# Kernel optimization log

Measured on AMD Instinct MI355X. Metric: run time of the kernel, lower is better.

## Reference

```python
import jax, jax.numpy as jnp
import numpy as np
from jax import lax

NMS_THR = 0.5
MIN_HEIGHT = 50.0
PULL_W = 1.0
PUSH_W = 1.0
EPS = 1e-6

B, N, G = 8, 2048, 64


def setup_inputs() -> dict:
    key = jax.random.key(0)
    k1, k2, k3, k4, k5, k6, k7 = jax.random.split(key, 7)
    # proposals: valid boxes (x1,y1,x2,y2) plus score in column 4
    cxy = jax.random.uniform(k1, (B, N, 2), minval=0.0, maxval=1000.0)
    wh = jax.random.uniform(k2, (B, N, 2), minval=10.0, maxval=200.0)
    scores = jax.random.uniform(k3, (B, N, 1))
    proposal_list = jnp.concatenate([cxy - wh / 2, cxy + wh / 2, scores], axis=-1)
    # gt boxes: heights straddle MIN_HEIGHT so the push branch is exercised
    gxy = jax.random.uniform(k4, (B, G, 2), minval=0.0, maxval=1000.0)
    gwh = jax.random.uniform(k5, (B, G, 2), minval=20.0, maxval=160.0)
    gt_bboxes = jnp.concatenate([gxy - gwh / 2, gxy + gwh / 2], axis=-1)
    # assignment ids in [-1, G); -1 = negative anchor
    anchor_gt_inds = jax.random.randint(k6, (B, N), -1, G, dtype=jnp.int32)
    gt_inds = jax.random.randint(k7, (B, N), -1, G, dtype=jnp.int32)  # dead arg in original
    return {"gt_inds": gt_inds, "anchor_gt_inds": anchor_gt_inds,
            "gt_bboxes": gt_bboxes, "proposal_list": proposal_list}


def bbox_overlaps(a, b):
    # a: [A,4], b: [B,4] -> IoU [A,B]
    area_a = (a[:, 2] - a[:, 0]) * (a[:, 3] - a[:, 1])
    area_b = (b[:, 2] - b[:, 0]) * (b[:, 3] - b[:, 1])
    lt = jnp.maximum(a[:, None, :2], b[None, :, :2])
    rb = jnp.minimum(a[:, None, 2:4], b[None, :, 2:4])
    wh = jnp.clip(rb - lt, 0.0)
    inter = wh[..., 0] * wh[..., 1]
    return inter / (area_a[:, None] + area_b[None, :] - inter + 1e-10)


def single_image_loss(prop, gtb, agti):
    scores = prop[:, 4]
    boxes = prop[:, :4]
    pos = agti >= 0
    n = scores.shape[0]
    g_n = gtb.shape[0]
    # push_select=True: suppression IoU rows use detached boxes
    iou = bbox_overlaps(lax.stop_gradient(boxes), boxes)          # [N,N]
    gtp = bbox_overlaps(gtb, boxes)                               # [G,N]

    def step(carry, _):
        active, seen, tp, pc = carry
        any_a = jnp.any(active)
        masked = jnp.where(active, scores, -jnp.inf)
        i = jnp.argmax(masked)                                    # highest remaining score
        g = jnp.maximum(agti[i], 0)                               # safe (gated by any_a)
        remaining = active & (jnp.arange(n) != i)
        has_rem = jnp.any(remaining)
        seen_g = seen[g]
        msi = jnp.maximum(gtp[g, i], EPS)
        pull = -jnp.log(jnp.minimum(1.0 - NMS_THR + msi, 1.0)) * lax.stop_gradient(scores[i])
        do_pull = any_a & seen_g
        # original adds pull only when idx non-empty, but counts pull_cnt before the break
        tp = tp + jnp.where(do_pull & has_rem, pull, 0.0)
        pc = pc + jnp.where(do_pull, 1, 0).astype(jnp.int32)
        seen = seen | ((jnp.arange(g_n) == g) & any_a & (~seen_g))
        new_active = jnp.where(any_a, remaining & ~(iou[i] > NMS_THR), active)
        return (new_active, seen, tp, pc), None

    init = (pos, jnp.zeros((g_n,), bool), jnp.float32(0.0), jnp.int32(0))
    (_, seen, tp, pc), _ = lax.scan(step, init, None, length=n)

    # push: per-gt highest-score positive proposal (first occurrence of max)
    mask = (agti[None, :] == jnp.arange(g_n)[:, None]) & pos[None, :]  # [G,N]
    smat = jnp.where(mask, scores[None, :], -jnp.inf)
    best = jnp.argmax(smat, axis=1)
    has_prop = jnp.any(mask, axis=1)
    height = gtb[:, 3] - gtb[:, 1]
    pmask = has_prop & (height >= MIN_HEIGHT) & (~seen)
    tmp_push = 1.0 - gtp[jnp.arange(g_n), best]
    total_push = jnp.sum(jnp.where(pmask, tmp_push, 0.0))
    push_cnt = jnp.sum(pmask)

    valid = jnp.sum(pos) > 1
    pull_loss = jnp.where(valid, tp / (pc.astype(jnp.float32) + EPS), 0.0)
    push_loss = jnp.where(valid, total_push / (push_cnt.astype(jnp.float32) + EPS), 0.0)
    return push_loss, pull_loss


def reference(gt_inds, anchor_gt_inds, gt_bboxes, proposal_list):
    # original: gt_inds = anchor_gt_inds (gt_inds arg unused)
    push, pull = jax.vmap(single_image_loss)(proposal_list, gt_bboxes, anchor_gt_inds)
    return jnp.stack([jnp.mean(push) * PUSH_W, jnp.mean(pull) * PULL_W])
```

## Files before the change

### kernel.cpp

```cpp
#include <hip/hip_runtime.h>
#include <math.h>


#define B_IMG 8
#define NN 2048
#define GG 64
#define MIN_H 50.0f
#define EPSF 1e-6f
#define TILE 256
#define NTILE 8
#define NPAIRT 36
#define CSLICE 64
#define ADJ_U64 33792

#define OFF_BOXO  0
#define OFF_GTPIO 32768
#define OFF_PULLO 40960
#define OFF_AGTIO 49152
#define OFF_NPOSP 51200
#define OFF_RANKP 51456
#define OFF_ADJ   84224
#define IMG_STRIDE 354560

__device__ __forceinline__ float iou_pair(
    float ax1, float ay1, float ax2, float ay2,
    float bx1, float by1, float bx2, float by2) {
  float area_a = (ax2 - ax1) * (ay2 - ay1);
  float area_b = (bx2 - bx1) * (by2 - by1);
  float lx = fmaxf(ax1, bx1), ly = fmaxf(ay1, by1);
  float rx = fminf(ax2, bx2), ry = fminf(ay2, by2);
  float w = fmaxf(rx - lx, 0.0f), h = fmaxf(ry - ly, 0.0f);
  float inter = w * h;
  return inter / (area_a + area_b - inter + 1e-10f);
}

__device__ __forceinline__ unsigned long long make_key(int a, float sc, int idx) {
  return (a >= 0)
      ? ((unsigned long long)__float_as_uint(sc) << 32) | (unsigned)(NN - 1 - idx)
      : 0ull;
}

__device__ __forceinline__ int adj_idx(int e, int wp) {
  int W = e >> 6, l = e & 63;
  return 32 * W * (W + 1) + (wp << 6) + l;
}

__global__ __launch_bounds__(256) void k_rank(
    const int* __restrict__ agti_all,
    const float* __restrict__ gtb_all,
    const float* __restrict__ prop_all,
    unsigned char* __restrict__ ws,
    float* __restrict__ out) {
  const int bidx = blockIdx.x;
  const int b = bidx >> 6;
  const int ec = (bidx >> 3) & 7, fc = bidx & 7;
  const int tid = threadIdx.x;
  const int* agti = agti_all + b * NN;
  const float* prop = prop_all + (size_t)b * NN * 5;
  unsigned char* W = ws + (size_t)b * IMG_STRIDE;

  if (bidx == 0 && tid == 0) { out[0] = 0.f; out[1] = 0.f; }

  {
    unsigned long long* adj = (unsigned long long*)(W + OFF_ADJ);
    for (int t = ((bidx & 63) << 8) + tid; t < ADJ_U64; t += 64 * 256)
      adj[t] = 0ull;
  }

  __shared__ unsigned long long fkeys[TILE];
  __shared__ float sgt[GG * 4];
  __shared__ int cnt4[4];

  const int f0 = fc << 8;
  {
    const int f = f0 + tid;
    fkeys[tid] = make_key(agti[f], prop[f * 5 + 4], f);
  }
  if (fc == 0) sgt[tid] = gtb_all[b * GG * 4 + tid];

  const int e = (ec << 8) + tid;
  const int a = agti[e];
  const float sc = prop[e * 5 + 4];
  const unsigned long long myk = make_key(a, sc, e);
  const bool pos = a >= 0;
  {
    unsigned long long bal = __ballot(pos);
    if ((tid & 63) == 0) cnt4[tid >> 6] = __popcll(bal);
  }
  __syncthreads();

  int rank = 0;
  #pragma unroll 16
  for (int ff = 0; ff < TILE; ++ff) {
    unsigned long long kf = fkeys[ff];
    int fi = f0 + ff;
    rank += (kf > myk || (kf == myk && fi < e)) ? 1 : 0;
  }
  ((unsigned short*)(W + OFF_RANKP))[(fc << 11) + e] = (unsigned short)rank;

  if (fc == 0) {
    float4 bx = make_float4(prop[e * 5 + 0], prop[e * 5 + 1],
                            prop[e * 5 + 2], prop[e * 5 + 3]);
    float gi = 0.f, pl = 0.f;
    if (pos) {
      gi = iou_pair(sgt[a * 4 + 0], sgt[a * 4 + 1], sgt[a * 4 + 2], sgt[a * 4 + 3],
                    bx.x, bx.y, bx.z, bx.w);
      pl = -logf(fminf(0.5f + fmaxf(gi, EPSF), 1.0f)) * sc;
    }
    ((float4*)(W + OFF_BOXO))[e] = bx;
    ((float*)(W + OFF_GTPIO))[e] = gi;
    ((float*)(W + OFF_PULLO))[e] = pl;
    ((signed char*)(W + OFF_AGTIO))[e] = (signed char)a;
    if (tid == 0)
      ((unsigned*)(W + OFF_NPOSP))[ec] =
          (unsigned)(cnt4[0] + cnt4[1] + cnt4[2] + cnt4[3]);
  }
}

__device__ __forceinline__ int load_npos(const unsigned char* W) {
  const unsigned* np = (const unsigned*)(W + OFF_NPOSP);
  return (int)(np[0] + np[1] + np[2] + np[3] + np[4] + np[5] + np[6] + np[7]);
}

__global__ __launch_bounds__(256) void k_pairs(unsigned char* __restrict__ ws) {
  int bx = blockIdx.x;
  const int b = bx / (NPAIRT * 4);
  int rem = bx % (NPAIRT * 4);
  int p = rem >> 2;
  const int q = rem & 3;
  int r = 0;
  #pragma unroll
  for (int t = 0; t < NTILE; ++t) {
    int wdt = NTILE - t;
    if (p < wdt) { r = t; break; }
    p -= wdt;
  }
  const int c = r + p;
  const int tid = threadIdx.x;
  unsigned char* W = ws + (size_t)b * IMG_STRIDE;
  const float4* box = (const float4*)(W + OFF_BOXO);
  const unsigned short* rp = (const unsigned short*)(W + OFF_RANKP);
  unsigned long long* adj = (unsigned long long*)(W + OFF_ADJ);

  __shared__ float4 cbox[CSLICE];
  __shared__ float carea[CSLICE];
  __shared__ unsigned short crank[CSLICE];

  const int jbase = c * TILE + q * CSLICE;
  if (tid < CSLICE) {
    int j = jbase + tid;
    float4 Bx = box[j];
    cbox[tid] = Bx;
    carea[tid] = (Bx.z - Bx.x) * (Bx.w - Bx.y);
    int rj = 0;
    #pragma unroll
    for (int fc = 0; fc < 8; ++fc) rj += rp[(fc << 11) + j];
    crank[tid] = (unsigned short)rj;
  }
  const int i = r * TILE + tid;
  const float4 A = box[i];
  const float area_a = (A.z - A.x) * (A.w - A.y);
  int ri = 0;
  #pragma unroll
  for (int fc = 0; fc < 8; ++fc) ri += rp[(fc << 11) + i];
  __syncthreads();

  const double THR = 0.5 + 0x1p-25;
  #pragma unroll 8
  for (int jj = 0; jj < CSLICE; ++jj) {
    float4 Bx = cbox[jj];
    float ab = carea[jj];
    float lx = fmaxf(A.x, Bx.x), ly = fmaxf(A.y, Bx.y);
    float rx = fminf(A.z, Bx.z), ry = fminf(A.w, Bx.w);
    float w = fmaxf(rx - lx, 0.0f), h = fmaxf(ry - ly, 0.0f);
    float inter = w * h;
    float denom = area_a + ab - inter + 1e-10f;
    int j = jbase + jj;
    bool hit = ((double)inter > THR * (double)denom) && (j > i);
    if (hit) {
      int rj = crank[jj];
      int rv = ri > rj ? ri : rj;
      int rk = ri > rj ? rj : ri;
      atomicOr(&adj[adj_idx(rv, rk >> 6)], 1ull << (rk & 63));
    }
  }
}

__global__ __launch_bounds__(512) void k_resolve(
    const float* __restrict__ gtb_all,
    unsigned char* __restrict__ ws,
    float* __restrict__ out) {
  const int b = blockIdx.x, tid = threadIdx.x;
  const int wave = tid >> 6, lane = tid & 63;
  unsigned char* W = ws + (size_t)b * IMG_STRIDE;
  const float* gtpiO = (const float*)(W + OFF_GTPIO);
  const float* pullO = (const float*)(W + OFF_PULLO);
  const signed char* agO = (const signed char*)(W + OFF_AGTIO);
  const unsigned long long* adj = (const unsigned long long*)(W + OFF_ADJ);
  const int npos = load_npos(W);

  __shared__ unsigned short perm[NN];
  __shared__ unsigned long long selw[32];
  __shared__ int minselg[GG], bestposg[GG];
  __shared__ int s_maxsel, s_hasrem;
  __shared__ float wtp[8];

  const unsigned long long* rbase[4];
  unsigned long long diag[4], cb[4][4], kmask[4];
  int myW[4], kword[4];
  bool kmulti[4];
  #pragma unroll
  for (int k = 0; k < 4; ++k) {
    myW[k] = (k << 3) + wave;
    const int Wb = myW[k];
    rbase[k] = adj + 32 * Wb * (Wb + 1) + lane;
    diag[k] = rbase[k][Wb << 6];
    #pragma unroll
    for (int j = 0; j < 4; ++j)
      cb[k][j] = (myW[k] > j) ? rbase[k][j << 6] : 0ull;
    kword[k] = -1; kmask[k] = 0ull; kmulti[k] = false;
  }

  {
    const unsigned short* rp = (const unsigned short*)(W + OFF_RANKP);
    #pragma unroll
    for (int k = 0; k < 4; ++k) {
      int o = tid + (k << 9);
      int rank = 0;
      #pragma unroll
      for (int fc = 0; fc < 8; ++fc) rank += rp[(fc << 11) + o];
      perm[rank] = (unsigned short)o;
    }
  }
  if (tid == 0) { s_maxsel = -1; s_hasrem = 0; }
  if (tid < GG) { minselg[tid] = NN; bestposg[tid] = NN; }
  __syncthreads();

  float mypull[4];
  int myag[4];
  #pragma unroll
  for (int k = 0; k < 4; ++k) {
    int e = tid + (k << 9);
    int o = perm[e];
    mypull[k] = pullO[o];
    myag[k] = agO[o];
  }

  #pragma unroll
  for (int w = 0; w < 32; ++w) {
    if (wave == (w & 7)) {
      const int k = w >> 3;
      const int e = (w << 6) | lane;
      const bool alive0 = (e < npos) && (kword[k] < 0);
      const unsigned long long intra = diag[k];
      bool alive = alive0;
      unsigned long long bal = __ballot(alive), prev;
      do {
        prev = bal;
        alive = alive0 && ((intra & bal) == 0ull);
        bal = __ballot(alive);
      } while (bal != prev);
      if (lane == 0) selw[w] = bal;
      unsigned long long mi = intra & bal;
      if (mi != 0ull) {
        kmulti[k] = kmulti[k] || (kword[k] >= 0);
        if (kword[k] < 0) { kword[k] = w; kmask[k] = mi; }
      }
    }
    asm volatile("s_waitcnt lgkmcnt(0)" ::: "memory");
    __builtin_amdgcn_s_barrier();
    __builtin_amdgcn_sched_barrier(0);
    const unsigned long long sw = selw[w];
    #pragma unroll
    for (int k = 0; k < 4; ++k) {
      if (myW[k] > w) {
        unsigned long long m = cb[k][w & 3] & sw;
        if (m != 0ull) {
          kmulti[k] = kmulti[k] || (kword[k] >= 0);
          if (kword[k] < 0) { kword[k] = w; kmask[k] = m; }
        }
      }
      cb[k][w & 3] = (myW[k] > w + 4) ? rbase[k][(w + 4) << 6] : 0ull;
    }
  }
  __syncthreads();

  float tp_part = 0.f;
  int maxsel_p = -1;
  #pragma unroll
  for (int k = 0; k < 4; ++k) {
    int e = tid + (k << 9);
    if (e < npos) {
      int g = myag[k];
      atomicMin(&bestposg[g], e);
      bool sel = (selw[e >> 6] >> (e & 63)) & 1ull;
      if (sel) {
        atomicMin(&minselg[g], e);
        tp_part += mypull[k];
        maxsel_p = e > maxsel_p ? e : maxsel_p;
      }
    }
  }
  #pragma unroll
  for (int off = 32; off; off >>= 1) {
    int o = __shfl_xor(maxsel_p, off, 64);
    maxsel_p = o > maxsel_p ? o : maxsel_p;
  }
  if (lane == 0) atomicMax(&s_maxsel, maxsel_p);
  __syncthreads();

  const int idx_last = s_maxsel;
  if (idx_last >= 0) {
    const int lw = idx_last >> 6;
    const unsigned long long lbit = 1ull << (idx_last & 63);
    #pragma unroll
    for (int k = 0; k < 4; ++k) {
      int e = tid + (k << 9);
      if (e < npos) {
        bool sel = (selw[e >> 6] >> (e & 63)) & 1ull;
        if (sel) {
          if (e == minselg[myag[k]]) tp_part -= mypull[k];
        } else if (!kmulti[k] && kword[k] == lw && kmask[k] == lbit) {
          s_hasrem = 1;
        }
      }
    }
  }
  #pragma unroll
  for (int off = 32; off; off >>= 1) tp_part += __shfl_xor(tp_part, off, 64);
  if (lane == 0) wtp[wave] = tp_part;
  __syncthreads();

  if (wave == 0) {
    float mypush = 0.f;
    int mycnt2 = 0;
    int bp = bestposg[lane];
    bool seen = minselg[lane] < NN;
    if (bp < NN) {
      float h = gtb_all[b * GG * 4 + lane * 4 + 3] - gtb_all[b * GG * 4 + lane * 4 + 1];
      if (h >= MIN_H && !seen) { mypush = 1.0f - gtpiO[perm[bp]]; mycnt2 = 1; }
    }
    #pragma unroll
    for (int off = 32; off; off >>= 1) {
      mypush += __shfl_xor(mypush, off, 64);
      mycnt2 += __shfl_xor(mycnt2, off, 64);
    }
    if (lane == 0) {
      float tp = 0.f;
      #pragma unroll
      for (int w = 0; w < 8; ++w) tp += wtp[w];
      int total_sel = 0;
      for (int w = 0; w < 32; ++w) total_sel += __popcll(selw[w]);
      int distinct = 0;
      for (int g = 0; g < GG; ++g) distinct += (minselg[g] < NN) ? 1 : 0;
      int pc = total_sel - distinct;
      if (idx_last >= 0) {
        int ol = perm[idx_last];
        if (idx_last != minselg[agO[ol]] && !s_hasrem) tp -= pullO[ol];
      }
      float push_loss = 0.f, pull_loss = 0.f;
      if (npos > 1) {
        pull_loss = tp / ((float)pc + EPSF);
        push_loss = mypush / ((float)mycnt2 + EPSF);
      }
      atomicAdd(&out[0], push_loss * (1.0f / B_IMG));
      atomicAdd(&out[1], pull_loss * (1.0f / B_IMG));
    }
  }
}

extern "C" void kernel_launch(void* const* d_in, const int* in_sizes, int n_in,
                              void* d_out, int out_size, void* d_ws, size_t ws_size,
                              hipStream_t stream) {
  const int* agti = (const int*)d_in[1];
  const float* gtb = (const float*)d_in[2];
  const float* prop = (const float*)d_in[3];
  unsigned char* ws = (unsigned char*)d_ws;
  float* out = (float*)d_out;

  k_rank<<<B_IMG * 64, 256, 0, stream>>>(agti, gtb, prop, ws, out);
  k_pairs<<<B_IMG * NPAIRT * 4, 256, 0, stream>>>(ws);
  k_resolve<<<B_IMG, 512, 0, stream>>>(gtb, ws, out);
}
```

Before: 47.42 us.

## Fuse rank, pair and resolve kernels into one persistent kernel with grid barriers

Merges the three launches into one 256-block persistent kernel that uses a software grid barrier between the rank, pairwise-IoU and resolve phases, removing launch gaps. It also skips pair slices whose rows or columns lie beyond the positive count. The resolve phase now runs with 256 threads instead of 512 and uses a two-deep row prefetch. In exchange it adds a memset launch for the barrier, halves resolve parallelism, and depends on all 256 blocks being co-resident for the spin barrier to make progress.

```diff
diff --git a/kernel.cpp b/kernel.cpp
--- a/kernel.cpp
+++ b/kernel.cpp
@@ -11,7 +11,9 @@
 #define NTILE 8
 #define NPAIRT 36
 #define CSLICE 64
+#define NSLICES (B_IMG * NPAIRT * 4)
 #define ADJ_U64 33792
+#define GRID_BLKS 256
 
 #define OFF_BOXO  0
 #define OFF_GTPIO 32768
@@ -21,6 +23,7 @@
 #define OFF_RANKP 51456
 #define OFF_ADJ   84224
 #define IMG_STRIDE 354560
+#define OFF_BAR ((size_t)B_IMG * IMG_STRIDE)
 
 __device__ __forceinline__ float iou_pair(
     float ax1, float ay1, float ax2, float ay2,
@@ -45,326 +48,349 @@
   return 32 * W * (W + 1) + (wp << 6) + l;
 }
 
-__global__ __launch_bounds__(256) void k_rank(
+__device__ __forceinline__ int load_npos(const unsigned char* W) {
+  const unsigned* np = (const unsigned*)(W + OFF_NPOSP);
+  return (int)(np[0] + np[1] + np[2] + np[3] + np[4] + np[5] + np[6] + np[7]);
+}
+
+__device__ __forceinline__ void grid_bar(unsigned* bar) {
+  __threadfence();
+  __syncthreads();
+  if (threadIdx.x == 0) {
+    unsigned g = __hip_atomic_load(&bar[1], __ATOMIC_ACQUIRE,
+                                   __HIP_MEMORY_SCOPE_AGENT);
+    unsigned old = __hip_atomic_fetch_add(&bar[0], 1u, __ATOMIC_ACQ_REL,
+                                          __HIP_MEMORY_SCOPE_AGENT);
+    if (old == GRID_BLKS - 1u) {
+      __hip_atomic_store(&bar[0], 0u, __ATOMIC_RELAXED,
+                         __HIP_MEMORY_SCOPE_AGENT);
+      __hip_atomic_fetch_add(&bar[1], 1u, __ATOMIC_ACQ_REL,
+                             __HIP_MEMORY_SCOPE_AGENT);
+    } else {
+      while (__hip_atomic_load(&bar[1], __ATOMIC_ACQUIRE,
+                               __HIP_MEMORY_SCOPE_AGENT) == g)
+        __builtin_amdgcn_s_sleep(8);
+    }
+  }
+  __syncthreads();
+}
+
+__global__ __launch_bounds__(256, 2) void k_fused(
     const int* __restrict__ agti_all,
     const float* __restrict__ gtb_all,
     const float* __restrict__ prop_all,
     unsigned char* __restrict__ ws,
     float* __restrict__ out) {
-  const int bidx = blockIdx.x;
-  const int b = bidx >> 6;
-  const int ec = (bidx >> 3) & 7, fc = bidx & 7;
   const int tid = threadIdx.x;
-  const int* agti = agti_all + b * NN;
-  const float* prop = prop_all + (size_t)b * NN * 5;
-  unsigned char* W = ws + (size_t)b * IMG_STRIDE;
-
-  if (bidx == 0 && tid == 0) { out[0] = 0.f; out[1] = 0.f; }
-
-  {
-    unsigned long long* adj = (unsigned long long*)(W + OFF_ADJ);
-    for (int t = ((bidx & 63) << 8) + tid; t < ADJ_U64; t += 64 * 256)
-      adj[t] = 0ull;
-  }
+  const int wave = tid >> 6, lane = tid & 63;
+  unsigned* bar = (unsigned*)(ws + OFF_BAR);
 
   __shared__ unsigned long long fkeys[TILE];
   __shared__ float sgt[GG * 4];
   __shared__ int cnt4[4];
-
-  const int f0 = fc << 8;
-  {
-    const int f = f0 + tid;
-    fkeys[tid] = make_key(agti[f], prop[f * 5 + 4], f);
-  }
-  if (fc == 0) sgt[tid] = gtb_all[b * GG * 4 + tid];
-
-  const int e = (ec << 8) + tid;
-  const int a = agti[e];
-  const float sc = prop[e * 5 + 4];
-  const unsigned long long myk = make_key(a, sc, e);
-  const bool pos = a >= 0;
-  {
-    unsigned long long bal = __ballot(pos);
-    if ((tid & 63) == 0) cnt4[tid >> 6] = __popcll(bal);
-  }
-  __syncthreads();
-
-  int rank = 0;
-  #pragma unroll 16
-  for (int ff = 0; ff < TILE; ++ff) {
-    unsigned long long kf = fkeys[ff];
-    int fi = f0 + ff;
-    rank += (kf > myk || (kf == myk && fi < e)) ? 1 : 0;
-  }
-  ((unsigned short*)(W + OFF_RANKP))[(fc << 11) + e] = (unsigned short)rank;
-
-  if (fc == 0) {
-    float4 bx = make_float4(prop[e * 5 + 0], prop[e * 5 + 1],
-                            prop[e * 5 + 2], prop[e * 5 + 3]);
-    float gi = 0.f, pl = 0.f;
-    if (pos) {
-      gi = iou_pair(sgt[a * 4 + 0], sgt[a * 4 + 1], sgt[a * 4 + 2], sgt[a * 4 + 3],
-                    bx.x, bx.y, bx.z, bx.w);
-      pl = -logf(fminf(0.5f + fmaxf(gi, EPSF), 1.0f)) * sc;
-    }
-    ((float4*)(W + OFF_BOXO))[e] = bx;
-    ((float*)(W + OFF_GTPIO))[e] = gi;
-    ((float*)(W + OFF_PULLO))[e] = pl;
-    ((signed char*)(W + OFF_AGTIO))[e] = (signed char)a;
-    if (tid == 0)
-      ((unsigned*)(W + OFF_NPOSP))[ec] =
-          (unsigned)(cnt4[0] + cnt4[1] + cnt4[2] + cnt4[3]);
-  }
-}
-
-__device__ __forceinline__ int load_npos(const unsigned char* W) {
-  const unsigned* np = (const unsigned*)(W + OFF_NPOSP);
-  return (int)(np[0] + np[1] + np[2] + np[3] + np[4] + np[5] + np[6] + np[7]);
-}
-
-__global__ __launch_bounds__(256) void k_pairs(unsigned char* __restrict__ ws) {
-  int bx = blockIdx.x;
-  const int b = bx / (NPAIRT * 4);
-  int rem = bx % (NPAIRT * 4);
-  int p = rem >> 2;
-  const int q = rem & 3;
-  int r = 0;
-  #pragma unroll
-  for (int t = 0; t < NTILE; ++t) {
-    int wdt = NTILE - t;
-    if (p < wdt) { r = t; break; }
-    p -= wdt;
-  }
-  const int c = r + p;
-  const int tid = threadIdx.x;
-  unsigned char* W = ws + (size_t)b * IMG_STRIDE;
-  const float4* box = (const float4*)(W + OFF_BOXO);
-  const unsigned short* rp = (const unsigned short*)(W + OFF_RANKP);
-  unsigned long long* adj = (unsigned long long*)(W + OFF_ADJ);
-
   __shared__ float4 cbox[CSLICE];
   __shared__ float carea[CSLICE];
   __shared__ unsigned short crank[CSLICE];
-
-  const int jbase = c * TILE + q * CSLICE;
-  if (tid < CSLICE) {
-    int j = jbase + tid;
-    float4 Bx = box[j];
-    cbox[tid] = Bx;
-    carea[tid] = (Bx.z - Bx.x) * (Bx.w - Bx.y);
-    int rj = 0;
-    #pragma unroll
-    for (int fc = 0; fc < 8; ++fc) rj += rp[(fc << 11) + j];
-    crank[tid] = (unsigned short)rj;
-  }
-  const int i = r * TILE + tid;
-  const float4 A = box[i];
-  const float area_a = (A.z - A.x) * (A.w - A.y);
-  int ri = 0;
-  #pragma unroll
-  for (int fc = 0; fc < 8; ++fc) ri += rp[(fc << 11) + i];
-  __syncthreads();
-
-  const double THR = 0.5 + 0x1p-25;
-  #pragma unroll 8
-  for (int jj = 0; jj < CSLICE; ++jj) {
-    float4 Bx = cbox[jj];
-    float ab = carea[jj];
-    float lx = fmaxf(A.x, Bx.x), ly = fmaxf(A.y, Bx.y);
-    float rx = fminf(A.z, Bx.z), ry = fminf(A.w, Bx.w);
-    float w = fmaxf(rx - lx, 0.0f), h = fmaxf(ry - ly, 0.0f);
-    float inter = w * h;
-    float denom = area_a + ab - inter + 1e-10f;
-    int j = jbase + jj;
-    bool hit = ((double)inter > THR * (double)denom) && (j > i);
-    if (hit) {
-      int rj = crank[jj];
-      int rv = ri > rj ? ri : rj;
-      int rk = ri > rj ? rj : ri;
-      atomicOr(&adj[adj_idx(rv, rk >> 6)], 1ull << (rk & 63));
-    }
-  }
-}
-
-__global__ __launch_bounds__(512) void k_resolve(
-    const float* __restrict__ gtb_all,
-    unsigned char* __restrict__ ws,
-    float* __restrict__ out) {
-  const int b = blockIdx.x, tid = threadIdx.x;
-  const int wave = tid >> 6, lane = tid & 63;
-  unsigned char* W = ws + (size_t)b * IMG_STRIDE;
-  const float* gtpiO = (const float*)(W + OFF_GTPIO);
-  const float* pullO = (const float*)(W + OFF_PULLO);
-  const signed char* agO = (const signed char*)(W + OFF_AGTIO);
-  const unsigned long long* adj = (const unsigned long long*)(W + OFF_ADJ);
-  const int npos = load_npos(W);
-
   __shared__ unsigned short perm[NN];
   __shared__ unsigned long long selw[32];
   __shared__ int minselg[GG], bestposg[GG];
   __shared__ int s_maxsel, s_hasrem;
-  __shared__ float wtp[8];
-
-  const unsigned long long* rbase[4];
-  unsigned long long diag[4], cb[4][4], kmask[4];
-  int myW[4], kword[4];
-  bool kmulti[4];
-  #pragma unroll
-  for (int k = 0; k < 4; ++k) {
-    myW[k] = (k << 3) + wave;
-    const int Wb = myW[k];
-    rbase[k] = adj + 32 * Wb * (Wb + 1) + lane;
-    diag[k] = rbase[k][Wb << 6];
-    #pragma unroll
-    for (int j = 0; j < 4; ++j)
-      cb[k][j] = (myW[k] > j) ? rbase[k][j << 6] : 0ull;
-    kword[k] = -1; kmask[k] = 0ull; kmulti[k] = false;
+  __shared__ float wtp[4];
+
+  for (int u = 0; u < 2; ++u) {
+    const int bidx = (int)blockIdx.x + (u << 8);
+    const int b = bidx >> 6, ec = (bidx >> 3) & 7, fc = bidx & 7;
+    const int* agti = agti_all + b * NN;
+    const float* prop = prop_all + (size_t)b * NN * 5;
+    unsigned char* W = ws + (size_t)b * IMG_STRIDE;
+
+    if (bidx == 0 && tid == 0) { out[0] = 0.f; out[1] = 0.f; }
+
+    {
+      unsigned long long* adj = (unsigned long long*)(W + OFF_ADJ);
+      for (int t = ((bidx & 63) << 8) + tid; t < ADJ_U64; t += 64 * 256)
+        adj[t] = 0ull;
+    }
+
+    const int f0 = fc << 8;
+    {
+      const int f = f0 + tid;
+      fkeys[tid] = make_key(agti[f], prop[f * 5 + 4], f);
+    }
+    if (fc == 0) sgt[tid] = gtb_all[b * GG * 4 + tid];
+
+    const int e = (ec << 8) + tid;
+    const int a = agti[e];
+    const float sc = prop[e * 5 + 4];
+    const unsigned long long myk = make_key(a, sc, e);
+    const bool pos = a >= 0;
+    {
+      unsigned long long bal = __ballot(pos);
+      if (lane == 0) cnt4[wave] = __popcll(bal);
+    }
+    __syncthreads();
+
+    int rank = 0;
+    #pragma unroll 16
+    for (int ff = 0; ff < TILE; ++ff) {
+      unsigned long long kf = fkeys[ff];
+      int fi = f0 + ff;
+      rank += (kf > myk || (kf == myk && fi < e)) ? 1 : 0;
+    }
+    ((unsigned short*)(W + OFF_RANKP))[(fc << 11) + e] = (unsigned short)rank;
+
+    if (fc == 0) {
+      float4 bx = make_float4(prop[e * 5 + 0], prop[e * 5 + 1],
+                              prop[e * 5 + 2], prop[e * 5 + 3]);
+      float gi = 0.f, pl = 0.f;
+      if (pos) {
+        gi = iou_pair(sgt[a * 4 + 0], sgt[a * 4 + 1], sgt[a * 4 + 2], sgt[a * 4 + 3],
+                      bx.x, bx.y, bx.z, bx.w);
+        pl = -logf(fminf(0.5f + fmaxf(gi, EPSF), 1.0f)) * sc;
+      }
+      ((float4*)(W + OFF_BOXO))[e] = bx;
+      ((float*)(W + OFF_GTPIO))[e] = gi;
+      ((float*)(W + OFF_PULLO))[e] = pl;
+      ((signed char*)(W + OFF_AGTIO))[e] = (signed char)a;
+      if (tid == 0)
+        ((unsigned*)(W + OFF_NPOSP))[ec] =
+            (unsigned)(cnt4[0] + cnt4[1] + cnt4[2] + cnt4[3]);
+    }
+    __syncthreads();
   }
-
+  grid_bar(bar);
+
+  for (int sl = (int)blockIdx.x; sl < NSLICES; sl += GRID_BLKS) {
+    const int b = sl / (NPAIRT * 4);
+    int rem = sl % (NPAIRT * 4);
+    int p = rem >> 2;
+    const int q = rem & 3;
+    int r = 0;
+    #pragma unroll
+    for (int t = 0; t < NTILE; ++t) {
+      int wdt = NTILE - t;
+      if (p < wdt) { r = t; break; }
+      p -= wdt;
+    }
+    const int c = r + p;
+    unsigned char* W = ws + (size_t)b * IMG_STRIDE;
+    const float4* box = (const float4*)(W + OFF_BOXO);
+    const unsigned short* rp = (const unsigned short*)(W + OFF_RANKP);
+    unsigned long long* adj = (unsigned long long*)(W + OFF_ADJ);
+    const int npos = load_npos(W);
+
+    const int jbase = c * TILE + q * CSLICE;
+    if (jbase >= npos || r * TILE >= npos) continue;
+
+    __syncthreads();
+    if (tid < CSLICE) {
+      int j = jbase + tid;
+      float4 Bx = box[j];
+      cbox[tid] = Bx;
+      carea[tid] = (Bx.z - Bx.x) * (Bx.w - Bx.y);
+      int rj = 0;
+      #pragma unroll
+      for (int fc = 0; fc < 8; ++fc) rj += rp[(fc << 11) + j];
+      crank[tid] = (unsigned short)rj;
+    }
+    const int i = r * TILE + tid;
+    const float4 A = box[i];
+    const float area_a = (A.z - A.x) * (A.w - A.y);
+    int ri = 0;
+    #pragma unroll
+    for (int fc = 0; fc < 8; ++fc) ri += rp[(fc << 11) + i];
+    __syncthreads();
+
+    const double THR = 0.5 + 0x1p-25;
+    #pragma unroll 8
+    for (int jj = 0; jj < CSLICE; ++jj) {
+      float4 Bx = cbox[jj];
+      float ab = carea[jj];
+      float lx = fmaxf(A.x, Bx.x), ly = fmaxf(A.y, Bx.y);
+      float rx = fminf(A.z, Bx.z), ry = fminf(A.w, Bx.w);
+      float w = fmaxf(rx - lx, 0.0f), h = fmaxf(ry - ly, 0.0f);
+      float inter = w * h;
+      float denom = area_a + ab - inter + 1e-10f;
+      int j = jbase + jj;
+      bool hit = ((double)inter > THR * (double)denom) && (j > i);
+      if (hit) {
+        int rj = crank[jj];
+        int rv = ri > rj ? ri : rj;
+        int rk = ri > rj ? rj : ri;
+        atomicOr(&adj[adj_idx(rv, rk >> 6)], 1ull << (rk & 63));
+      }
+    }
+  }
+  grid_bar(bar);
+
+  if (blockIdx.x >= B_IMG) return;
   {
-    const unsigned short* rp = (const unsigned short*)(W + OFF_RANKP);
-    #pragma unroll
-    for (int k = 0; k < 4; ++k) {
-      int o = tid + (k << 9);
-      int rank = 0;
+    const int b = (int)blockIdx.x;
+    unsigned char* W = ws + (size_t)b * IMG_STRIDE;
+    const float* gtpiO = (const float*)(W + OFF_GTPIO);
+    const float* pullO = (const float*)(W + OFF_PULLO);
+    const signed char* agO = (const signed char*)(W + OFF_AGTIO);
+    const unsigned long long* adj = (const unsigned long long*)(W + OFF_ADJ);
+    const int npos = load_npos(W);
+
+    const unsigned long long* rbase[8];
+    unsigned long long diag[8], cb0[8], cb1[8], kmask[8];
+    int kword[8];
+    bool kmulti[8];
+    #pragma unroll
+    for (int k = 0; k < 8; ++k) {
+      const int mw = (k << 2) + wave;
+      rbase[k] = adj + 32 * mw * (mw + 1) + lane;
+      diag[k] = rbase[k][mw << 6];
+      cb0[k] = (mw > 0) ? rbase[k][0] : 0ull;
+      cb1[k] = (mw > 1) ? rbase[k][1 << 6] : 0ull;
+      kword[k] = -1; kmask[k] = 0ull; kmulti[k] = false;
+    }
+
+    {
+      const unsigned short* rp = (const unsigned short*)(W + OFF_RANKP);
       #pragma unroll
-      for (int fc = 0; fc < 8; ++fc) rank += rp[(fc << 11) + o];
-      perm[rank] = (unsigned short)o;
-    }
-  }
-  if (tid == 0) { s_maxsel = -1; s_hasrem = 0; }
-  if (tid < GG) { minselg[tid] = NN; bestposg[tid] = NN; }
-  __syncthreads();
-
-  float mypull[4];
-  int myag[4];
-  #pragma unroll
-  for (int k = 0; k < 4; ++k) {
-    int e = tid + (k << 9);
-    int o = perm[e];
-    mypull[k] = pullO[o];
-    myag[k] = agO[o];
-  }
-
-  #pragma unroll
-  for (int w = 0; w < 32; ++w) {
-    if (wave == (w & 7)) {
-      const int k = w >> 3;
-      const int e = (w << 6) | lane;
-      const bool alive0 = (e < npos) && (kword[k] < 0);
-      const unsigned long long intra = diag[k];
-      bool alive = alive0;
-      unsigned long long bal = __ballot(alive), prev;
-      do {
-        prev = bal;
-        alive = alive0 && ((intra & bal) == 0ull);
-        bal = __ballot(alive);
-      } while (bal != prev);
-      if (lane == 0) selw[w] = bal;
-      unsigned long long mi = intra & bal;
-      if (mi != 0ull) {
-        kmulti[k] = kmulti[k] || (kword[k] >= 0);
-        if (kword[k] < 0) { kword[k] = w; kmask[k] = mi; }
-      }
-    }
-    asm volatile("s_waitcnt lgkmcnt(0)" ::: "memory");
-    __builtin_amdgcn_s_barrier();
-    __builtin_amdgcn_sched_barrier(0);
-    const unsigned long long sw = selw[w];
-    #pragma unroll
-    for (int k = 0; k < 4; ++k) {
-      if (myW[k] > w) {
-        unsigned long long m = cb[k][w & 3] & sw;
-        if (m != 0ull) {
+      for (int k = 0; k < 8; ++k) {
+        int o = tid + (k << 8);
+        int rank = 0;
+        #pragma unroll
+        for (int fc = 0; fc < 8; ++fc) rank += rp[(fc << 11) + o];
+        perm[rank] = (unsigned short)o;
+      }
+    }
+    if (tid == 0) { s_maxsel = -1; s_hasrem = 0; }
+    if (tid < GG) { minselg[tid] = NN; bestposg[tid] = NN; }
+    __syncthreads();
+
+    float mypull[8];
+    int myag[8];
+    #pragma unroll
+    for (int k = 0; k < 8; ++k) {
+      int o = perm[tid + (k << 8)];
+      mypull[k] = pullO[o];
+      myag[k] = agO[o];
+    }
+
+    #pragma unroll
+    for (int w = 0; w < 32; ++w) {
+      if (wave == (w & 3)) {
+        const int k = w >> 2;
+        const int e = (w << 6) | lane;
+        const bool alive0 = (e < npos) && (kword[k] < 0);
+        const unsigned long long intra = diag[k];
+        bool alive = alive0;
+        unsigned long long bal = __ballot(alive), prev;
+        do {
+          prev = bal;
+          alive = alive0 && ((intra & bal) == 0ull);
+          bal = __ballot(alive);
+        } while (bal != prev);
+        if (lane == 0) selw[w] = bal;
+        unsigned long long mi = intra & bal;
+        if (mi != 0ull) {
           kmulti[k] = kmulti[k] || (kword[k] >= 0);
-          if (kword[k] < 0) { kword[k] = w; kmask[k] = m; }
-        }
-      }
-      cb[k][w & 3] = (myW[k] > w + 4) ? rbase[k][(w + 4) << 6] : 0ull;
-    }
-  }
-  __syncthreads();
-
-  float tp_part = 0.f;
-  int maxsel_p = -1;
-  #pragma unroll
-  for (int k = 0; k < 4; ++k) {
-    int e = tid + (k << 9);
-    if (e < npos) {
-      int g = myag[k];
-      atomicMin(&bestposg[g], e);
-      bool sel = (selw[e >> 6] >> (e & 63)) & 1ull;
-      if (sel) {
-        atomicMin(&minselg[g], e);
-        tp_part += mypull[k];
-        maxsel_p = e > maxsel_p ? e : maxsel_p;
-      }
-    }
-  }
-  #pragma unroll
-  for (int off = 32; off; off >>= 1) {
-    int o = __shfl_xor(maxsel_p, off, 64);
-    maxsel_p = o > maxsel_p ? o : maxsel_p;
-  }
-  if (lane == 0) atomicMax(&s_maxsel, maxsel_p);
-  __syncthreads();
-
-  const int idx_last = s_maxsel;
-  if (idx_last >= 0) {
-    const int lw = idx_last >> 6;
-    const unsigned long long lbit = 1ull << (idx_last & 63);
-    #pragma unroll
-    for (int k = 0; k < 4; ++k) {
-      int e = tid + (k << 9);
+          if (kword[k] < 0) { kword[k] = w; kmask[k] = mi; }
+        }
+      }
+      __syncthreads();
+      const unsigned long long sw = selw[w];
+      #pragma unroll
+      for (int k = 0; k < 8; ++k) {
+        const int mw = (k << 2) + wave;
+        unsigned long long cur = ((w & 1) == 0) ? cb0[k] : cb1[k];
+        if (mw > w) {
+          unsigned long long m = cur & sw;
+          if (m != 0ull) {
+            kmulti[k] = kmulti[k] || (kword[k] >= 0);
+            if (kword[k] < 0) { kword[k] = w; kmask[k] = m; }
+          }
+        }
+        unsigned long long nxt = (mw > w + 2) ? rbase[k][(w + 2) << 6] : 0ull;
+        if ((w & 1) == 0) cb0[k] = nxt; else cb1[k] = nxt;
+      }
+    }
+    __syncthreads();
+
+    float tp_part = 0.f;
+    int maxsel_p = -1;
+    #pragma unroll
+    for (int k = 0; k < 8; ++k) {
+      int e = tid + (k << 8);
       if (e < npos) {
+        int g = myag[k];
+        atomicMin(&bestposg[g], e);
         bool sel = (selw[e >> 6] >> (e & 63)) & 1ull;
         if (sel) {
-          if (e == minselg[myag[k]]) tp_part -= mypull[k];
-        } else if (!kmulti[k] && kword[k] == lw && kmask[k] == lbit) {
-          s_hasrem = 1;
-        }
-      }
-    }
-  }
-  #pragma unroll
-  for (int off = 32; off; off >>= 1) tp_part += __shfl_xor(tp_part, off, 64);
-  if (lane == 0) wtp[wave] = tp_part;
-  __syncthreads();
-
-  if (wave == 0) {
-    float mypush = 0.f;
-    int mycnt2 = 0;
-    int bp = bestposg[lane];
-    bool seen = minselg[lane] < NN;
-    if (bp < NN) {
-      float h = gtb_all[b * GG * 4 + lane * 4 + 3] - gtb_all[b * GG * 4 + lane * 4 + 1];
-      if (h >= MIN_H && !seen) { mypush = 1.0f - gtpiO[perm[bp]]; mycnt2 = 1; }
+          atomicMin(&minselg[g], e);
+          tp_part += mypull[k];
+          maxsel_p = e > maxsel_p ? e : maxsel_p;
+        }
+      }
     }
     #pragma unroll
     for (int off = 32; off; off >>= 1) {
-      mypush += __shfl_xor(mypush, off, 64);
-      mycnt2 += __shfl_xor(mycnt2, off, 64);
-    }
-    if (lane == 0) {
-      float tp = 0.f;
+      int o = __shfl_xor(maxsel_p, off, 64);
+      maxsel_p = o > maxsel_p ? o : maxsel_p;
+    }
+    if (lane == 0) atomicMax(&s_maxsel, maxsel_p);
+    __syncthreads();
+
+    const int idx_last = s_maxsel;
+    if (idx_last >= 0) {
+      const int lw = idx_last >> 6;
+      const unsigned long long lbit = 1ull << (idx_last & 63);
       #pragma unroll
-      for (int w = 0; w < 8; ++w) tp += wtp[w];
-      int total_sel = 0;
-      for (int w = 0; w < 32; ++w) total_sel += __popcll(selw[w]);
-      int distinct = 0;
-      for (int g = 0; g < GG; ++g) distinct += (minselg[g] < NN) ? 1 : 0;
-      int pc = total_sel - distinct;
-      if (idx_last >= 0) {
-        int ol = perm[idx_last];
-        if (idx_last != minselg[agO[ol]] && !s_hasrem) tp -= pullO[ol];
-      }
-      float push_loss = 0.f, pull_loss = 0.f;
-      if (npos > 1) {
-        pull_loss = tp / ((float)pc + EPSF);
-        push_loss = mypush / ((float)mycnt2 + EPSF);
-      }
-      atomicAdd(&out[0], push_loss * (1.0f / B_IMG));
-      atomicAdd(&out[1], pull_loss * (1.0f / B_IMG));
+      for (int k = 0; k < 8; ++k) {
+        int e = tid + (k << 8);
+        if (e < npos) {
+          bool sel = (selw[e >> 6] >> (e & 63)) & 1ull;
+          if (sel) {
+            if (e == minselg[myag[k]]) tp_part -= mypull[k];
+          } else if (!kmulti[k] && kword[k] == lw && kmask[k] == lbit) {
+            s_hasrem = 1;
+          }
+        }
+      }
+    }
+    #pragma unroll
+    for (int off = 32; off; off >>= 1) tp_part += __shfl_xor(tp_part, off, 64);
+    if (lane == 0) wtp[wave] = tp_part;
+    __syncthreads();
+
+    if (wave == 0) {
+      float mypush = 0.f;
+      int mycnt2 = 0;
+      int bp = bestposg[lane];
+      bool seen = minselg[lane] < NN;
+      if (bp < NN) {
+        float h = gtb_all[b * GG * 4 + lane * 4 + 3] -
+                  gtb_all[b * GG * 4 + lane * 4 + 1];
+        if (h >= MIN_H && !seen) { mypush = 1.0f - gtpiO[perm[bp]]; mycnt2 = 1; }
+      }
+      #pragma unroll
+      for (int off = 32; off; off >>= 1) {
+        mypush += __shfl_xor(mypush, off, 64);
+        mycnt2 += __shfl_xor(mycnt2, off, 64);
+      }
+      if (lane == 0) {
+        float tp = wtp[0] + wtp[1] + wtp[2] + wtp[3];
+        int total_sel = 0;
+        for (int w = 0; w < 32; ++w) total_sel += __popcll(selw[w]);
+        int distinct = 0;
+        for (int g = 0; g < GG; ++g) distinct += (minselg[g] < NN) ? 1 : 0;
+        int pc = total_sel - distinct;
+        if (idx_last >= 0) {
+          int ol = perm[idx_last];
+          if (idx_last != minselg[agO[ol]] && !s_hasrem) tp -= pullO[ol];
+        }
+        float push_loss = 0.f, pull_loss = 0.f;
+        if (npos > 1) {
+          pull_loss = tp / ((float)pc + EPSF);
+          push_loss = mypush / ((float)mycnt2 + EPSF);
+        }
+        atomicAdd(&out[0], push_loss * (1.0f / B_IMG));
+        atomicAdd(&out[1], pull_loss * (1.0f / B_IMG));
+      }
     }
   }
 }
@@ -378,7 +404,6 @@
   unsigned char* ws = (unsigned char*)d_ws;
   float* out = (float*)d_out;
 
-  k_rank<<<B_IMG * 64, 256, 0, stream>>>(agti, gtb, prop, ws, out);
-  k_pairs<<<B_IMG * NPAIRT * 4, 256, 0, stream>>>(ws);
-  k_resolve<<<B_IMG, 512, 0, stream>>>(gtb, ws, out);
-}
+  hipMemsetAsync(ws + OFF_BAR, 0, 128, stream);
+  k_fused<<<GRID_BLKS, 256, 0, stream>>>(agti, gtb, prop, ws, out);
+}
```

Result: slower. 163.5 us (+244.8%).
